# Optimization experiments

Hardware: AMD Instinct MI355X
Metric: run time of the kernel (lower is better)

## Reference

```python
import jax, jax.numpy as jnp
import numpy as np

H = 8           # hidden_size
IN = 1          # input_size
OUT = 1         # output_size
T_IN = 512      # input_length
T_OUT = 128     # output_length
B = 65536       # batch


def _gru_cell(x, h, W_ih, W_hh, b_ih, b_hh):
    # torch.nn.GRUCell math. x: [B, D], h: [B, H]
    gi = x @ W_ih.T + b_ih          # [B, 3H]
    gh = h @ W_hh.T + b_hh          # [B, 3H]
    i_r, i_z, i_n = jnp.split(gi, 3, axis=-1)
    h_r, h_z, h_n = jnp.split(gh, 3, axis=-1)
    r = jax.nn.sigmoid(i_r + h_r)
    z = jax.nn.sigmoid(i_z + h_z)
    n = jnp.tanh(i_n + r * h_n)
    return (1.0 - z) * n + z * h


def setup_inputs() -> dict:
    key = jax.random.key(0)
    ks = jax.random.split(key, 12)
    s_in = 1.0 / np.sqrt(H)
    x = jax.random.normal(ks[0], (T_IN, B, IN), dtype=jnp.float32)
    u = lambda k, shp: jax.random.uniform(k, shp, dtype=jnp.float32, minval=-s_in, maxval=s_in)
    return {
        "x": x,
        "enc_W_ih": u(ks[1], (3 * H, IN)),
        "enc_W_hh": u(ks[2], (3 * H, H)),
        "enc_b_ih": u(ks[3], (3 * H,)),
        "enc_b_hh": u(ks[4], (3 * H,)),
        "dec_W_ih": u(ks[5], (3 * H, OUT)),
        "dec_W_hh": u(ks[6], (3 * H, H)),
        "dec_b_ih": u(ks[7], (3 * H,)),
        "dec_b_hh": u(ks[8], (3 * H,)),
        "fc_W": u(ks[9], (OUT, H)),
        "fc_b": u(ks[10], (OUT,)),
    }


def reference(x, enc_W_ih, enc_W_hh, enc_b_ih, enc_b_hh,
              dec_W_ih, dec_W_hh, dec_b_ih, dec_b_hh, fc_W, fc_b):
    batch = x.shape[1]
    h0 = jnp.zeros((batch, H), dtype=x.dtype)

    def enc_step(h, x_t):
        return _gru_cell(x_t, h, enc_W_ih, enc_W_hh, enc_b_ih, enc_b_hh), None

    enc_h, _ = jax.lax.scan(enc_step, h0, x)

    def dec_step(carry, _):
        h, inp = carry
        h = _gru_cell(inp, h, dec_W_ih, dec_W_hh, dec_b_ih, dec_b_hh)
        out_t = h @ fc_W.T + fc_b      # [B, OUT]
        return (h, out_t), out_t

    # decoder_feat is None, teacher_forcing False: feed back own prediction
    _, outs = jax.lax.scan(dec_step, (enc_h, x[-1]), None, length=T_OUT)
    return outs  # [T_OUT, B, OUT]
```

## Files before the change

kernel.cpp:

```cpp
#include <hip/hip_runtime.h>

#define T_IN   512
#define T_OUT  128
#define BATCH  65536

typedef float v2f __attribute__((ext_vector_type(2)));
typedef float v4f __attribute__((ext_vector_type(4)));

__device__ __forceinline__ float exp2_fast(float v) { return __builtin_amdgcn_exp2f(v); }
__device__ __forceinline__ float rcp_fast(float v)  { return __builtin_amdgcn_rcpf(v); }

__global__ __launch_bounds__(256) void gru_seq2seq(
    const float* __restrict__ x,
    const float* __restrict__ eWih, const float* __restrict__ eWhh,
    const float* __restrict__ eBih, const float* __restrict__ eBhh,
    const float* __restrict__ dWih, const float* __restrict__ dWhh,
    const float* __restrict__ dBih, const float* __restrict__ dBhh,
    const float* __restrict__ fcW,  const float* __restrict__ fcB,
    float* __restrict__ out)
{
    __shared__ __align__(16) float hsh[32][8];
    const int tid = threadIdx.x;
    const int k   = tid & 7;
    const int el  = tid >> 3;
    const int e   = (int)blockIdx.x * 32 + el;

    const float CR = -1.44269504088896340736f;
    const float CN =  2.88539008177792681472f;

    v2f wr[4], wz[4], wn[4];
    float wir, wiz, win, bbr, bbz, binS, bhnS;

    auto load_w = [&](const float* Wih, const float* Whh,
                      const float* Bih, const float* Bhh) {
        #pragma unroll
        for (int p = 0; p < 4; ++p) {
            wr[p] = v2f{ Whh[k*8      + 2*p] * CR, Whh[k*8      + 2*p + 1] * CR };
            wz[p] = v2f{ Whh[(k+8)*8  + 2*p] * CR, Whh[(k+8)*8  + 2*p + 1] * CR };
            wn[p] = v2f{ Whh[(k+16)*8 + 2*p] * CN, Whh[(k+16)*8 + 2*p + 1] * CN };
        }
        wir = Wih[k]    * CR;  wiz = Wih[k+8] * CR;  win = Wih[k+16] * CN;
        bbr = (Bih[k]   + Bhh[k])   * CR;
        bbz = (Bih[k+8] + Bhh[k+8]) * CR;
        binS = Bih[k+16] * CN;
        bhnS = Bhh[k+16] * CN;
    };

    load_w(eWih, eWhh, eBih, eBhh);

    float h = 0.0f;
    v4f hva = {0.f, 0.f, 0.f, 0.f};
    v4f hvb = {0.f, 0.f, 0.f, 0.f};

    auto cell = [&](float xin) {
        v2f h01 = __builtin_shufflevector(hva, hva, 0, 1);
        v2f h23 = __builtin_shufflevector(hva, hva, 2, 3);
        v2f h45 = __builtin_shufflevector(hvb, hvb, 0, 1);
        v2f h67 = __builtin_shufflevector(hvb, hvb, 2, 3);

        v2f ar = v2f{ bbr,  0.f };
        v2f az = v2f{ bbz,  0.f };
        v2f an = v2f{ bhnS, 0.f };
        ar = __builtin_elementwise_fma(wr[0], h01, ar);
        az = __builtin_elementwise_fma(wz[0], h01, az);
        an = __builtin_elementwise_fma(wn[0], h01, an);
        ar = __builtin_elementwise_fma(wr[1], h23, ar);
        az = __builtin_elementwise_fma(wz[1], h23, az);
        an = __builtin_elementwise_fma(wn[1], h23, an);
        ar = __builtin_elementwise_fma(wr[2], h45, ar);
        az = __builtin_elementwise_fma(wz[2], h45, az);
        an = __builtin_elementwise_fma(wn[2], h45, an);
        ar = __builtin_elementwise_fma(wr[3], h67, ar);
        az = __builtin_elementwise_fma(wz[3], h67, az);
        an = __builtin_elementwise_fma(wn[3], h67, an);

        const float sr = fmaf(xin, wir, ar.x + ar.y);
        const float sz = fmaf(xin, wiz, az.x + az.y);
        const float hn = an.x + an.y;

        const float er = exp2_fast(sr);
        const float ez = exp2_fast(sz);
        const float dr = 1.0f + er;
        const float dz = 1.0f + ez;
        const float rp = rcp_fast(dr * dz);
        const float r  = dz * rp;
        const float z  = dr * rp;

        float pre = fmaf(xin, win, binS);
        pre = fmaf(r, hn, pre);
        const float en = exp2_fast(pre);
        const float rn = rcp_fast(1.0f + en);
        const float n  = fmaf(-2.0f, rn, 1.0f);

        h = fmaf(z, h - n, n);

        hsh[el][k] = h;
        asm volatile("" ::: "memory");
        hva = *(const v4f*)&hsh[el][0];
        hvb = *(const v4f*)&hsh[el][4];
        asm volatile("" ::: "memory");
    };

    const float* xp = x + e;
    float x0 = xp[0];
    float x1 = xp[BATCH];
    xp += 2 * (size_t)BATCH;
    #pragma unroll 1
    for (int t = 0; t < T_IN - 2; ++t) {
        const float x2 = *xp; xp += BATCH;
        cell(x0);
        x0 = x1; x1 = x2;
    }
    cell(x0);
    cell(x1);

    load_w(dWih, dWhh, dBih, dBhh);
    v2f fw2[4];
    #pragma unroll
    for (int p = 0; p < 4; ++p) fw2[p] = v2f{ fcW[2*p], fcW[2*p+1] };
    const float fb = fcB[0];

    float inp = x1;
    float* outp = out + e;
    #pragma unroll 1
    for (int t = 0; t < T_OUT; ++t) {
        cell(inp);
        v2f h01 = __builtin_shufflevector(hva, hva, 0, 1);
        v2f h23 = __builtin_shufflevector(hva, hva, 2, 3);
        v2f h45 = __builtin_shufflevector(hvb, hvb, 0, 1);
        v2f h67 = __builtin_shufflevector(hvb, hvb, 2, 3);
        v2f ay = v2f{ fb, 0.f };
        ay = __builtin_elementwise_fma(fw2[0], h01, ay);
        ay = __builtin_elementwise_fma(fw2[1], h23, ay);
        ay = __builtin_elementwise_fma(fw2[2], h45, ay);
        ay = __builtin_elementwise_fma(fw2[3], h67, ay);
        const float y = ay.x + ay.y;
        if (k == 0) outp[t * BATCH] = y;
        inp = y;
    }
}

extern "C" void kernel_launch(void* const* d_in, const int* in_sizes, int n_in,
                              void* d_out, int out_size, void* d_ws, size_t ws_size,
                              hipStream_t stream) {
    const float* x    = (const float*)d_in[0];
    const float* eWih = (const float*)d_in[1];
    const float* eWhh = (const float*)d_in[2];
    const float* eBih = (const float*)d_in[3];
    const float* eBhh = (const float*)d_in[4];
    const float* dWih = (const float*)d_in[5];
    const float* dWhh = (const float*)d_in[6];
    const float* dBih = (const float*)d_in[7];
    const float* dBhh = (const float*)d_in[8];
    const float* fcW  = (const float*)d_in[9];
    const float* fcB  = (const float*)d_in[10];
    float* out = (float*)d_out;

    dim3 grid(BATCH / 32);
    dim3 block(256);
    gru_seq2seq<<<grid, block, 0, stream>>>(x, eWih, eWhh, eBih, eBhh,
                                            dWih, dWhh, dBih, dBhh,
                                            fcW, fcB, out);
}
```

Measured before the change: 418.1 us.

## Replace LDS hidden-state exchange with DPP lane permutes in GRU cell

Each step now broadcasts the 8-wide hidden state among the 8 lanes of a batch element with DPP quad-permute and row-half-mirror moves instead of writing to LDS and reading it back. The recurrent weights are pre-permuted by XOR lane index so each lane's dot product matches its permuted copy of the hidden state. The change also adds an occupancy hint to launch bounds and unrolls the encoder loop by two. The aim is to take LDS latency off the serial recurrence, at the cost of correctness depending on the DPP lane mappings being right.

```diff
diff --git a/kernel.cpp b/kernel.cpp
--- a/kernel.cpp
+++ b/kernel.cpp
@@ -5,12 +5,20 @@
 #define BATCH  65536
 
 typedef float v2f __attribute__((ext_vector_type(2)));
-typedef float v4f __attribute__((ext_vector_type(4)));
 
 __device__ __forceinline__ float exp2_fast(float v) { return __builtin_amdgcn_exp2f(v); }
 __device__ __forceinline__ float rcp_fast(float v)  { return __builtin_amdgcn_rcpf(v); }
 
-__global__ __launch_bounds__(256) void gru_seq2seq(
+template<int CTRL>
+__device__ __forceinline__ float dppf(float v) {
+    return __int_as_float(__builtin_amdgcn_mov_dpp(__float_as_int(v), CTRL, 0xF, 0xF, false));
+}
+#define QP_XOR1 0xB1
+#define QP_XOR2 0x4E
+#define QP_XOR3 0x1B
+#define HALF_MIRROR 0x141
+
+__global__ __launch_bounds__(256, 8) void gru_seq2seq(
     const float* __restrict__ x,
     const float* __restrict__ eWih, const float* __restrict__ eWhh,
     const float* __restrict__ eBih, const float* __restrict__ eBhh,
@@ -19,51 +27,42 @@
     const float* __restrict__ fcW,  const float* __restrict__ fcB,
     float* __restrict__ out)
 {
-    __shared__ __align__(16) float hsh[32][8];
     const int tid = threadIdx.x;
-    const int k   = tid & 7;
-    const int el  = tid >> 3;
-    const int e   = (int)blockIdx.x * 32 + el;
+    const int u   = tid & 7;
+    const int e   = (int)blockIdx.x * 32 + (tid >> 3);
 
     const float CR = -1.44269504088896340736f;
     const float CN =  2.88539008177792681472f;
 
     v2f wr[4], wz[4], wn[4];
-    float wir, wiz, win, bbr, bbz, binS, bhnS;
+    v2f brv, bzv, bnv;
+    float wir, wiz, win, binS;
 
     auto load_w = [&](const float* Wih, const float* Whh,
                       const float* Bih, const float* Bhh) {
         #pragma unroll
         for (int p = 0; p < 4; ++p) {
-            wr[p] = v2f{ Whh[k*8      + 2*p] * CR, Whh[k*8      + 2*p + 1] * CR };
-            wz[p] = v2f{ Whh[(k+8)*8  + 2*p] * CR, Whh[(k+8)*8  + 2*p + 1] * CR };
-            wn[p] = v2f{ Whh[(k+16)*8 + 2*p] * CN, Whh[(k+16)*8 + 2*p + 1] * CN };
+            const int c0 = u ^ (2*p), c1 = u ^ (2*p + 1);
+            wr[p] = v2f{ Whh[u*8      + c0] * CR, Whh[u*8      + c1] * CR };
+            wz[p] = v2f{ Whh[(u+8)*8  + c0] * CR, Whh[(u+8)*8  + c1] * CR };
+            wn[p] = v2f{ Whh[(u+16)*8 + c0] * CN, Whh[(u+16)*8 + c1] * CN };
         }
-        wir = Wih[k]    * CR;  wiz = Wih[k+8] * CR;  win = Wih[k+16] * CN;
-        bbr = (Bih[k]   + Bhh[k])   * CR;
-        bbz = (Bih[k+8] + Bhh[k+8]) * CR;
-        binS = Bih[k+16] * CN;
-        bhnS = Bhh[k+16] * CN;
+        wir = Wih[u]    * CR;  wiz = Wih[u+8] * CR;  win = Wih[u+16] * CN;
+        brv = v2f{ (Bih[u]   + Bhh[u])   * CR, 0.f };
+        bzv = v2f{ (Bih[u+8] + Bhh[u+8]) * CR, 0.f };
+        bnv = v2f{ Bhh[u+16] * CN,             0.f };
+        binS = Bih[u+16] * CN;
     };
 
     load_w(eWih, eWhh, eBih, eBhh);
 
     float h = 0.0f;
-    v4f hva = {0.f, 0.f, 0.f, 0.f};
-    v4f hvb = {0.f, 0.f, 0.f, 0.f};
+    v2f h01 = {0.f,0.f}, h23 = {0.f,0.f}, h45 = {0.f,0.f}, h67 = {0.f,0.f};
 
     auto cell = [&](float xin) {
-        v2f h01 = __builtin_shufflevector(hva, hva, 0, 1);
-        v2f h23 = __builtin_shufflevector(hva, hva, 2, 3);
-        v2f h45 = __builtin_shufflevector(hvb, hvb, 0, 1);
-        v2f h67 = __builtin_shufflevector(hvb, hvb, 2, 3);
-
-        v2f ar = v2f{ bbr,  0.f };
-        v2f az = v2f{ bbz,  0.f };
-        v2f an = v2f{ bhnS, 0.f };
-        ar = __builtin_elementwise_fma(wr[0], h01, ar);
-        az = __builtin_elementwise_fma(wz[0], h01, az);
-        an = __builtin_elementwise_fma(wn[0], h01, an);
+        v2f ar = __builtin_elementwise_fma(wr[0], h01, brv);
+        v2f az = __builtin_elementwise_fma(wz[0], h01, bzv);
+        v2f an = __builtin_elementwise_fma(wn[0], h01, bnv);
         ar = __builtin_elementwise_fma(wr[1], h23, ar);
         az = __builtin_elementwise_fma(wz[1], h23, az);
         an = __builtin_elementwise_fma(wn[1], h23, an);
@@ -94,18 +93,21 @@
 
         h = fmaf(z, h - n, n);
 
-        hsh[el][k] = h;
-        asm volatile("" ::: "memory");
-        hva = *(const v4f*)&hsh[el][0];
-        hvb = *(const v4f*)&hsh[el][4];
-        asm volatile("" ::: "memory");
+        h01.x = h;
+        h01.y = dppf<QP_XOR1>(h);
+        h23.x = dppf<QP_XOR2>(h);
+        h23.y = dppf<QP_XOR1>(h23.x);
+        h67.y = dppf<HALF_MIRROR>(h);
+        h67.x = dppf<QP_XOR1>(h67.y);
+        h45.y = dppf<QP_XOR2>(h67.y);
+        h45.x = dppf<QP_XOR3>(h67.y);
     };
 
     const float* xp = x + e;
     float x0 = xp[0];
     float x1 = xp[BATCH];
     xp += 2 * (size_t)BATCH;
-    #pragma unroll 1
+    #pragma unroll 2
     for (int t = 0; t < T_IN - 2; ++t) {
         const float x2 = *xp; xp += BATCH;
         cell(x0);
@@ -115,27 +117,23 @@
     cell(x1);
 
     load_w(dWih, dWhh, dBih, dBhh);
-    v2f fw2[4];
+    v2f fw[4];
     #pragma unroll
-    for (int p = 0; p < 4; ++p) fw2[p] = v2f{ fcW[2*p], fcW[2*p+1] };
-    const float fb = fcB[0];
+    for (int p = 0; p < 4; ++p)
+        fw[p] = v2f{ fcW[u ^ (2*p)], fcW[u ^ (2*p + 1)] };
+    const v2f fbv = v2f{ fcB[0], 0.f };
 
     float inp = x1;
     float* outp = out + e;
     #pragma unroll 1
     for (int t = 0; t < T_OUT; ++t) {
         cell(inp);
-        v2f h01 = __builtin_shufflevector(hva, hva, 0, 1);
-        v2f h23 = __builtin_shufflevector(hva, hva, 2, 3);
-        v2f h45 = __builtin_shufflevector(hvb, hvb, 0, 1);
-        v2f h67 = __builtin_shufflevector(hvb, hvb, 2, 3);
-        v2f ay = v2f{ fb, 0.f };
-        ay = __builtin_elementwise_fma(fw2[0], h01, ay);
-        ay = __builtin_elementwise_fma(fw2[1], h23, ay);
-        ay = __builtin_elementwise_fma(fw2[2], h45, ay);
-        ay = __builtin_elementwise_fma(fw2[3], h67, ay);
+        v2f ay = __builtin_elementwise_fma(fw[0], h01, fbv);
+        ay = __builtin_elementwise_fma(fw[1], h23, ay);
+        ay = __builtin_elementwise_fma(fw[2], h45, ay);
+        ay = __builtin_elementwise_fma(fw[3], h67, ay);
         const float y = ay.x + ay.y;
-        if (k == 0) outp[t * BATCH] = y;
+        if (u == 0) outp[t * BATCH] = y;
         inp = y;
     }
 }
```

After: 438.1 us. +4.8%, slower.
